# Optimization experiments

Hardware: AMD Instinct MI355X
Metric: run time of the kernel (lower is better)

Reference implementation:

```python
import jax, jax.numpy as jnp
import numpy as np

N_NODES = 100000
N_EDGES = 1600000
FEAT = 128
HID = 128
CLS = 4


def setup_inputs() -> dict:
    key = jax.random.key(0)
    ks = jax.random.split(key, 10)
    x = jax.random.normal(ks[0], (N_NODES, FEAT), dtype=jnp.float32)
    edge_index = jax.random.randint(ks[1], (2, N_EDGES), 0, N_NODES, dtype=jnp.int64)
    s1 = 1.0 / np.sqrt(FEAT)
    s2 = 1.0 / np.sqrt(HID)
    s3 = 1.0 / np.sqrt(CLS)
    return {
        "x": x,
        "edge_index": edge_index,
        "W1l": jax.random.uniform(ks[2], (HID, FEAT), jnp.float32, -s1, s1),
        "b1": jax.random.uniform(ks[3], (HID,), jnp.float32, -s1, s1),
        "W1r": jax.random.uniform(ks[4], (HID, FEAT), jnp.float32, -s1, s1),
        "W2l": jax.random.uniform(ks[5], (CLS, HID), jnp.float32, -s2, s2),
        "b2": jax.random.uniform(ks[6], (CLS,), jnp.float32, -s2, s2),
        "W2r": jax.random.uniform(ks[7], (CLS, HID), jnp.float32, -s2, s2),
        "Wlin": jax.random.uniform(ks[8], (2, CLS), jnp.float32, -s3, s3),
        "blin": jax.random.uniform(ks[9], (2,), jnp.float32, -s3, s3),
    }


def _sage_conv(h, src, dst, Wl, bl, Wr, n_nodes):
    # PyG SAGEConv (mean aggr, root_weight=True): lin_l(mean_j h_j) + lin_r(h_i)
    msg = h[src]  # [E, d] irregular gather
    agg = jax.ops.segment_sum(msg, dst, num_segments=n_nodes)  # [N, d]
    deg = jax.ops.segment_sum(jnp.ones((src.shape[0], 1), h.dtype), dst,
                              num_segments=n_nodes)  # [N, 1]
    agg = agg / jnp.maximum(deg, 1.0)
    return agg @ Wl.T + bl + h @ Wr.T


def reference(x, edge_index, W1l, b1, W1r, W2l, b2, W2r, Wlin, blin):
    n = x.shape[0]
    src, dst = edge_index[0], edge_index[1]
    h = jax.nn.relu(_sage_conv(x, src, dst, W1l, b1, W1r, n))
    # dropout is identity in eval mode (training=False)
    h = _sage_conv(h, src, dst, W2l, b2, W2r, n)  # [N, 4]
    return h @ Wlin.T + blin  # [N, 2]
```

## Files before the change

### kernel.cpp

```cpp
#include <hip/hip_runtime.h>

#define NN 100000
#define NE 1600000
#define NBUK 1563
#define EB 8192

typedef __attribute__((ext_vector_type(8))) short v8s;
typedef __attribute__((ext_vector_type(4))) float v4f;

__device__ __forceinline__ unsigned short f2bf(float f) {
  unsigned int u = __float_as_uint(f);
  unsigned int r = (u + 0x7FFFu + ((u >> 16) & 1u)) >> 16;
  return (unsigned short)r;
}
__device__ __forceinline__ float bflo(unsigned int w) { return __uint_as_float(w << 16); }
__device__ __forceinline__ float bfhi(unsigned int w) { return __uint_as_float(w & 0xFFFF0000u); }
__device__ __forceinline__ float bf2f(unsigned short w) {
  return __uint_as_float((unsigned int)w << 16);
}


__global__ void k_zerob(int* __restrict__ hist) {
  int i = blockIdx.x * blockDim.x + threadIdx.x;
  if (i < NBUK) hist[i] = 0;
}

__global__ __launch_bounds__(256) void k_hist(const int* __restrict__ dst,
                                              int* __restrict__ hist) {
  __shared__ int lh[NBUK];
  int t = threadIdx.x;
  for (int i = t; i < NBUK; i += 256) lh[i] = 0;
  __syncthreads();
  int base = blockIdx.x * 16384;
  int lim = min(16384, NE - base);
  for (int j = t; j < lim; j += 256) atomicAdd(&lh[dst[base + j] >> 6], 1);
  __syncthreads();
  for (int i = t; i < NBUK; i += 256) {
    int c = lh[i];
    if (c) atomicAdd(&hist[i], c);
  }
}

__global__ __launch_bounds__(256) void k_scanb(const int* __restrict__ hist,
                                               int* __restrict__ bbase,
                                               int* __restrict__ gcur) {
  __shared__ int sc[256];
  __shared__ int carry;
  int t = threadIdx.x;
  if (t == 0) carry = 0;
  __syncthreads();
  for (int c = 0; c < (NBUK + 255) / 256; ++c) {
    int i = c * 256 + t;
    int vv = (i < NBUK) ? hist[i] : 0;
    sc[t] = vv;
    __syncthreads();
    for (int o = 1; o < 256; o <<= 1) {
      int uu = (t >= o) ? sc[t - o] : 0;
      __syncthreads();
      sc[t] += uu;
      __syncthreads();
    }
    int excl = carry + sc[t] - vv;
    if (i < NBUK) { bbase[i] = excl; gcur[i] = excl; }
    __syncthreads();
    if (t == 0) carry += sc[255];
    __syncthreads();
  }
}

extern __shared__ char smem_dyn[];
__global__ __launch_bounds__(256) void k_scatter(const int* __restrict__ src,
                                                 const int* __restrict__ dst,
                                                 int* __restrict__ gcur,
                                                 unsigned int* __restrict__ staged) {
  unsigned int* stageP = (unsigned int*)smem_dyn;
  unsigned short* stageB = (unsigned short*)(stageP + EB);
  int* lhist  = (int*)(stageB + EB);
  int* lbase  = lhist + NBUK;
  int* lcur   = lbase + NBUK;
  int* gclaim = lcur + NBUK;
  __shared__ int sc[256];
  __shared__ int carry;
  int t = threadIdx.x;
  int e0 = blockIdx.x * EB;
  int ecnt = min(EB, NE - e0);
  for (int i = t; i < NBUK; i += 256) lhist[i] = 0;
  if (t == 0) carry = 0;
  __syncthreads();
  for (int j = t; j < ecnt; j += 256) atomicAdd(&lhist[dst[e0 + j] >> 6], 1);
  __syncthreads();
  for (int c = 0; c < (NBUK + 255) / 256; ++c) {
    int i = c * 256 + t;
    int vv = (i < NBUK) ? lhist[i] : 0;
    sc[t] = vv;
    __syncthreads();
    for (int o = 1; o < 256; o <<= 1) {
      int uu = (t >= o) ? sc[t - o] : 0;
      __syncthreads();
      sc[t] += uu;
      __syncthreads();
    }
    int excl = carry + sc[t] - vv;
    if (i < NBUK) { lbase[i] = excl; lcur[i] = excl; }
    __syncthreads();
    if (t == 0) carry += sc[255];
    __syncthreads();
  }
  for (int b = t; b < NBUK; b += 256) {
    int c = lhist[b];
    gclaim[b] = c ? atomicAdd(&gcur[b], c) : 0;
  }
  __syncthreads();
  for (int j = t; j < ecnt; j += 256) {
    int s = src[e0 + j], d = dst[e0 + j];
    int b = d >> 6;
    int lp = atomicAdd(&lcur[b], 1);
    stageP[lp] = ((unsigned int)s << 6) | (unsigned int)(d & 63);
    stageB[lp] = (unsigned short)b;
  }
  __syncthreads();
  for (int i = t; i < ecnt; i += 256) {
    int b = stageB[i];
    staged[gclaim[b] + (i - lbase[b])] = stageP[i];
  }
}

__global__ __launch_bounds__(256) void k_sort2(const unsigned int* __restrict__ staged,
                                               const int* __restrict__ bbase,
                                               const int* __restrict__ hist,
                                               int* __restrict__ csr,
                                               int* __restrict__ off,
                                               int* __restrict__ deg) {
  __shared__ int h64[64], c64[64];
  int bkt = blockIdx.x, t = threadIdx.x;
  if (t < 64) h64[t] = 0;
  __syncthreads();
  int st = bbase[bkt], cnt = hist[bkt];
  for (int j = t; j < cnt; j += 256) atomicAdd(&h64[staged[st + j] & 63], 1);
  __syncthreads();
  if (t < 64) {
    int v = h64[t];
    int inc = v;
    for (int o = 1; o < 64; o <<= 1) {
      int uu = __shfl_up(inc, o, 64);
      if (t >= o) inc += uu;
    }
    int excl = inc - v;
    c64[t] = excl;
    int node = bkt * 64 + t;
    if (node < NN) { off[node] = st + excl; deg[node] = v; }
  }
  __syncthreads();
  for (int j = t; j < cnt; j += 256) {
    unsigned pk = staged[st + j];
    int lp = atomicAdd(&c64[pk & 63], 1);
    csr[st + lp] = (int)(pk >> 6);
  }
}


__global__ void k_packw(const float* __restrict__ W1l, const float* __restrict__ W1r,
                        unsigned short* __restrict__ Wcat) {
  int i = blockIdx.x * blockDim.x + threadIdx.x;
  float f = (i < 16384) ? W1l[i] : W1r[i - 16384];
  Wcat[i] = f2bf(f);
}

__global__ __launch_bounds__(256) void k_gemm1(
    const float* __restrict__ x, const unsigned short* __restrict__ Wcat,
    unsigned short* __restrict__ u, unsigned short* __restrict__ v) {
  int wave = threadIdx.x >> 6, l = threadIdx.x & 63;
  int m0 = blockIdx.x * 64 + wave * 16;
  if (m0 >= NN) return;
  int lr = l & 15, kq = l >> 4;
  int rowc = min(m0 + lr, NN - 1);

  v8s a[4];
#pragma unroll
  for (int ks = 0; ks < 4; ++ks) {
    const float* xp = x + (size_t)rowc * 128 + ks * 32 + kq * 8;
    float4 f0 = *(const float4*)xp;
    float4 f1 = *(const float4*)(xp + 4);
    v8s tv;
    tv[0] = (short)f2bf(f0.x); tv[1] = (short)f2bf(f0.y);
    tv[2] = (short)f2bf(f0.z); tv[3] = (short)f2bf(f0.w);
    tv[4] = (short)f2bf(f1.x); tv[5] = (short)f2bf(f1.y);
    tv[6] = (short)f2bf(f1.z); tv[7] = (short)f2bf(f1.w);
    a[ks] = tv;
  }

  v4f acc[16];
#pragma unroll
  for (int nt = 0; nt < 16; ++nt) acc[nt] = (v4f){0.f, 0.f, 0.f, 0.f};

#pragma unroll
  for (int nt = 0; nt < 16; ++nt) {
    const unsigned short* wrow = Wcat + (size_t)(nt * 16 + lr) * 128;
#pragma unroll
    for (int ks = 0; ks < 4; ++ks) {
      v8s b = *(const v8s*)(wrow + ks * 32 + kq * 8);
      acc[nt] = __builtin_amdgcn_mfma_f32_16x16x32_bf16(a[ks], b, acc[nt], 0, 0, 0);
    }
  }

#pragma unroll
  for (int nt = 0; nt < 16; ++nt) {
#pragma unroll
    for (int rr = 0; rr < 4; ++rr) {
      int mrow = m0 + kq * 4 + rr;
      if (mrow < NN) {
        unsigned short bv = f2bf(acc[nt][rr]);
        int col = nt * 16 + lr;
        if (nt < 8) u[(size_t)mrow * 128 + col] = bv;
        else        v[(size_t)mrow * 128 + (col - 128)] = bv;
      }
    }
  }
}

__global__ __launch_bounds__(256) void k_agg(
    const unsigned short* __restrict__ u, const unsigned short* __restrict__ v,
    const int* __restrict__ csr, const int* __restrict__ off, const int* __restrict__ deg,
    const float* __restrict__ b1,
    const float* __restrict__ W2l, const float* __restrict__ W2r,
    float* __restrict__ p, float* __restrict__ r) {
  int wid = (blockIdx.x * blockDim.x + threadIdx.x) >> 6;
  int l = threadIdx.x & 63;
  if (wid >= NN) return;
  int cnt = deg[wid], st = off[wid];
  int half = l >> 5;
  int dpos = l & 31;
  const char* ubase = (const char*)u + (dpos << 3);

  uint2 vw = *(const uint2*)((const char*)v + ((size_t)wid << 8) + (dpos << 3));
  float4 bb = *(const float4*)(b1 + 4 * dpos);
  const float* Wbase = half ? W2r : W2l;
  float4 wv[4];
#pragma unroll
  for (int o = 0; o < 4; ++o) wv[o] = *(const float4*)(Wbase + o * 128 + 4 * dpos);

  float a0 = 0.f, a1 = 0.f, a2 = 0.f, a3 = 0.f;

#define LOADW(W, S) uint2 W = *(const uint2*)(ubase + ((size_t)((unsigned)(S) << 8)))
#define ACCW(W) { a0 += bflo(W.x); a1 += bfhi(W.x); a2 += bflo(W.y); a3 += bfhi(W.y); }

  for (int base = 0; base < cnt; base += 64) {
    int nloc = min(64, cnt - base);
    int idx = 0;
    if (l < nloc) idx = csr[st + base + l];
    int npair = nloc >> 1;
    int e = 0;
    for (; e + 8 <= npair; e += 8) {
      int s0 = __shfl(idx, 2 * e + half, 64);
      int s1 = __shfl(idx, 2 * (e + 1) + half, 64);
      int s2 = __shfl(idx, 2 * (e + 2) + half, 64);
      int s3 = __shfl(idx, 2 * (e + 3) + half, 64);
      int s4 = __shfl(idx, 2 * (e + 4) + half, 64);
      int s5 = __shfl(idx, 2 * (e + 5) + half, 64);
      int s6 = __shfl(idx, 2 * (e + 6) + half, 64);
      int s7 = __shfl(idx, 2 * (e + 7) + half, 64);
      LOADW(w0, s0);
      LOADW(w1, s1);
      LOADW(w2, s2);
      LOADW(w3, s3);
      LOADW(w4, s4);
      LOADW(w5, s5);
      LOADW(w6, s6);
      LOADW(w7, s7);
      ACCW(w0); ACCW(w1); ACCW(w2); ACCW(w3);
      ACCW(w4); ACCW(w5); ACCW(w6); ACCW(w7);
    }
    for (; e + 4 <= npair; e += 4) {
      int s0 = __shfl(idx, 2 * e + half, 64);
      int s1 = __shfl(idx, 2 * (e + 1) + half, 64);
      int s2 = __shfl(idx, 2 * (e + 2) + half, 64);
      int s3 = __shfl(idx, 2 * (e + 3) + half, 64);
      LOADW(w0, s0);
      LOADW(w1, s1);
      LOADW(w2, s2);
      LOADW(w3, s3);
      ACCW(w0); ACCW(w1); ACCW(w2); ACCW(w3);
    }
    for (; e < npair; ++e) {
      int s = __shfl(idx, 2 * e + half, 64);
      LOADW(w, s);
      ACCW(w);
    }
    if (nloc & 1) {
      int s = __shfl(idx, nloc - 1, 64);
      if (half == 0) {
        LOADW(w, s);
        ACCW(w);
      }
    }
  }
#undef LOADW
#undef ACCW

  a0 += __shfl_xor(a0, 32, 64);
  a1 += __shfl_xor(a1, 32, 64);
  a2 += __shfl_xor(a2, 32, 64);
  a3 += __shfl_xor(a3, 32, 64);

  float inv = 1.f / (float)max(cnt, 1);
  float h0 = fmaxf(fmaf(a0, inv, bflo(vw.x) + bb.x), 0.f);
  float h1 = fmaxf(fmaf(a1, inv, bfhi(vw.x) + bb.y), 0.f);
  float h2 = fmaxf(fmaf(a2, inv, bflo(vw.y) + bb.z), 0.f);
  float h3 = fmaxf(fmaf(a3, inv, bfhi(vw.y) + bb.w), 0.f);

  float t0 = h0 * wv[0].x + h1 * wv[0].y + h2 * wv[0].z + h3 * wv[0].w;
  float t1 = h0 * wv[1].x + h1 * wv[1].y + h2 * wv[1].z + h3 * wv[1].w;
  float t2 = h0 * wv[2].x + h1 * wv[2].y + h2 * wv[2].z + h3 * wv[2].w;
  float t3 = h0 * wv[3].x + h1 * wv[3].y + h2 * wv[3].z + h3 * wv[3].w;
  float v01 = (l & 1) ? t1 : t0;
  float w01 = __shfl_xor((l & 1) ? t0 : t1, 1, 64);
  float r01 = v01 + w01;
  float v23 = (l & 1) ? t3 : t2;
  float w23 = __shfl_xor((l & 1) ? t2 : t3, 1, 64);
  float r23 = v23 + w23;
  float vq = (l & 2) ? r23 : r01;
  float wq = __shfl_xor((l & 2) ? r01 : r23, 2, 64);
  float rr = vq + wq;
  rr += __shfl_xor(rr, 4, 64);
  rr += __shfl_xor(rr, 8, 64);
  rr += __shfl_xor(rr, 16, 64);
  float* outp = half ? r : p;
  if (dpos < 4) outp[(size_t)wid * 4 + dpos] = rr;
}

__global__ __launch_bounds__(256) void k_final(
    const float* __restrict__ p, const float* __restrict__ r,
    const int* __restrict__ csr, const int* __restrict__ off,
    const int* __restrict__ deg,
    const float* __restrict__ b2,
    const float* __restrict__ Wlin, const float* __restrict__ blin,
    float* __restrict__ out) {
  int gid = blockIdx.x * blockDim.x + threadIdx.x;
  int node = gid >> 3;
  int sl = gid & 7;
  if (node >= NN) return;
  int cnt = deg[node], st = off[node];
  int l = threadIdx.x & 63;

  float a0 = 0.f, a1 = 0.f, a2 = 0.f, a3 = 0.f;
  for (int e = sl; e < cnt; e += 8) {
    int s = csr[st + e];
    const float4 pv = *(const float4*)(p + (size_t)s * 4);
    a0 += pv.x; a1 += pv.y; a2 += pv.z; a3 += pv.w;
  }
  float v01 = (l & 1) ? a1 : a0;
  float w01 = __shfl_xor((l & 1) ? a0 : a1, 1, 64);
  float r01 = v01 + w01;
  float v23 = (l & 1) ? a3 : a2;
  float w23 = __shfl_xor((l & 1) ? a2 : a3, 1, 64);
  float r23 = v23 + w23;
  float vq = (l & 2) ? r23 : r01;
  float wq = __shfl_xor((l & 2) ? r01 : r23, 2, 64);
  float rr = vq + wq;
  rr += __shfl_xor(rr, 4, 64);
  int o = sl & 3;
  float inv = 1.f / (float)max(cnt, 1);
  float g = rr * inv + b2[o] + r[(size_t)node * 4 + o];
  float t0 = g * Wlin[o];
  float t1 = g * Wlin[4 + o];
  float vv = (l & 1) ? t1 : t0;
  float ww = __shfl_xor((l & 1) ? t0 : t1, 1, 64);
  float q = vv + ww;
  q += __shfl_xor(q, 2, 64);
  if (sl < 2) out[(size_t)node * 2 + sl] = q + blin[sl];
}


extern "C" void kernel_launch(void* const* d_in, const int* in_sizes, int n_in,
                              void* d_out, int out_size, void* d_ws, size_t ws_size,
                              hipStream_t stream) {
  const float* x    = (const float*)d_in[0];
  const int*   ei   = (const int*)d_in[1];
  const int*   src  = ei;
  const int*   dst  = ei + NE;
  const float* W1l  = (const float*)d_in[2];
  const float* b1   = (const float*)d_in[3];
  const float* W1r  = (const float*)d_in[4];
  const float* W2l  = (const float*)d_in[5];
  const float* b2   = (const float*)d_in[6];
  const float* W2r  = (const float*)d_in[7];
  const float* Wlin = (const float*)d_in[8];
  const float* blin = (const float*)d_in[9];
  float* out = (float*)d_out;

  char* w = (char*)d_ws;
  size_t o = 0;
  auto alloc = [&](size_t bytes) {
    void* pp = (void*)(w + o);
    o = (o + bytes + 255) & ~(size_t)255;
    return pp;
  };
  int* hist  = (int*)alloc(NBUK * 4);
  int* bbase = (int*)alloc(NBUK * 4);
  int* gcur  = (int*)alloc(NBUK * 4);
  unsigned int*  staged = (unsigned int*)alloc((size_t)NE * 4);
  int* csr   = (int*)alloc((size_t)NE * 4);
  int* offs  = (int*)alloc(NN * 4);
  int* deg   = (int*)alloc(NN * 4);
  unsigned short* Wcat  = (unsigned short*)alloc(256 * 128 * 2);
  unsigned short* ubuf  = (unsigned short*)alloc((size_t)NN * 128 * 2);
  unsigned short* vbuf  = (unsigned short*)alloc((size_t)NN * 128 * 2);
  float* pbuf = (float*)alloc((size_t)NN * 4 * 4);
  float* rbuf = (float*)alloc((size_t)NN * 4 * 4);

  const size_t scatter_lds = (size_t)EB * 4 + (size_t)EB * 2 + (size_t)4 * NBUK * 4;

  hipLaunchKernelGGL(k_zerob, dim3((NBUK + 255) / 256), dim3(256), 0, stream, hist);
  hipLaunchKernelGGL(k_hist,  dim3((NE + 16383) / 16384), dim3(256), 0, stream, dst, hist);
  hipLaunchKernelGGL(k_scanb, dim3(1), dim3(256), 0, stream, hist, bbase, gcur);
  hipLaunchKernelGGL(k_scatter, dim3((NE + EB - 1) / EB), dim3(256), scatter_lds, stream,
                     src, dst, gcur, staged);
  hipLaunchKernelGGL(k_sort2, dim3(NBUK), dim3(256), 0, stream,
                     staged, bbase, hist, csr, offs, deg);
  hipLaunchKernelGGL(k_packw, dim3(128), dim3(256), 0, stream, W1l, W1r, Wcat);
  hipLaunchKernelGGL(k_gemm1, dim3((NN + 63) / 64), dim3(256), 0, stream, x, Wcat, ubuf, vbuf);
  hipLaunchKernelGGL(k_agg,   dim3((NN * 64 + 255) / 256), dim3(256), 0, stream,
                     ubuf, vbuf, csr, offs, deg, b1, W2l, W2r, pbuf, rbuf);
  hipLaunchKernelGGL(k_final, dim3((NN * 8 + 255) / 256), dim3(256), 0, stream,
                     pbuf, rbuf, csr, offs, deg, b2, Wlin, blin, out);
}
```

Measured before the change: 317.8 us.

## Stage W in LDS for gemm1 and swap MFMA operands for vector stores

The first-layer GEMM now copies the packed 256x128 bf16 weight matrix into padded shared memory once per block, instead of having every wave read it from global memory. The MFMA operands are swapped so each lane holds four consecutive output columns of one row. This lets results be written as packed 8-byte stores rather than scattered 2-byte stores. The cost is about 68KB of LDS per block, which limits occupancy, plus a block barrier; the early return for out-of-range waves is removed.

Result: faster. 281.0 us (-11.6%).

```diff
diff --git a/kernel.cpp b/kernel.cpp
--- a/kernel.cpp
+++ b/kernel.cpp
@@ -169,9 +169,20 @@
 __global__ __launch_bounds__(256) void k_gemm1(
     const float* __restrict__ x, const unsigned short* __restrict__ Wcat,
     unsigned short* __restrict__ u, unsigned short* __restrict__ v) {
-  int wave = threadIdx.x >> 6, l = threadIdx.x & 63;
+  char* wlds = smem_dyn;
+  int t = threadIdx.x;
+  {
+    int rsub = t >> 4, chunk = t & 15;
+#pragma unroll
+    for (int rd = 0; rd < 16; ++rd) {
+      int row = rd * 16 + rsub;
+      uint4 w4 = *(const uint4*)(Wcat + (size_t)row * 128 + chunk * 8);
+      *(uint4*)(wlds + row * 272 + chunk * 16) = w4;
+    }
+  }
+
+  int wave = t >> 6, l = t & 63;
   int m0 = blockIdx.x * 64 + wave * 16;
-  if (m0 >= NN) return;
   int lr = l & 15, kq = l >> 4;
   int rowc = min(m0 + lr, NN - 1);
 
@@ -189,31 +200,31 @@
     a[ks] = tv;
   }
 
+  __syncthreads();
+
   v4f acc[16];
 #pragma unroll
   for (int nt = 0; nt < 16; ++nt) acc[nt] = (v4f){0.f, 0.f, 0.f, 0.f};
 
 #pragma unroll
   for (int nt = 0; nt < 16; ++nt) {
-    const unsigned short* wrow = Wcat + (size_t)(nt * 16 + lr) * 128;
+    const char* wrow = wlds + (nt * 16 + lr) * 272;
 #pragma unroll
     for (int ks = 0; ks < 4; ++ks) {
-      v8s b = *(const v8s*)(wrow + ks * 32 + kq * 8);
-      acc[nt] = __builtin_amdgcn_mfma_f32_16x16x32_bf16(a[ks], b, acc[nt], 0, 0, 0);
-    }
-  }
-
-#pragma unroll
-  for (int nt = 0; nt < 16; ++nt) {
-#pragma unroll
-    for (int rr = 0; rr < 4; ++rr) {
-      int mrow = m0 + kq * 4 + rr;
-      if (mrow < NN) {
-        unsigned short bv = f2bf(acc[nt][rr]);
-        int col = nt * 16 + lr;
-        if (nt < 8) u[(size_t)mrow * 128 + col] = bv;
-        else        v[(size_t)mrow * 128 + (col - 128)] = bv;
-      }
+      v8s b = *(const v8s*)(wrow + ks * 64 + kq * 16);
+      acc[nt] = __builtin_amdgcn_mfma_f32_16x16x32_bf16(b, a[ks], acc[nt], 0, 0, 0);
+    }
+  }
+
+  if (m0 + lr < NN) {
+    size_t rowb = (size_t)(m0 + lr) * 128;
+#pragma unroll
+    for (int nt = 0; nt < 16; ++nt) {
+      unsigned lo = (unsigned)f2bf(acc[nt][0]) | ((unsigned)f2bf(acc[nt][1]) << 16);
+      unsigned hi = (unsigned)f2bf(acc[nt][2]) | ((unsigned)f2bf(acc[nt][3]) << 16);
+      int col = (nt & 7) * 16 + kq * 4;
+      if (nt < 8) *(uint2*)(u + rowb + col) = make_uint2(lo, hi);
+      else        *(uint2*)(v + rowb + col) = make_uint2(lo, hi);
     }
   }
 }
@@ -409,6 +420,7 @@
   float* rbuf = (float*)alloc((size_t)NN * 4 * 4);
 
   const size_t scatter_lds = (size_t)EB * 4 + (size_t)EB * 2 + (size_t)4 * NBUK * 4;
+  const size_t gemm1_lds = 256 * 272;
 
   hipLaunchKernelGGL(k_zerob, dim3((NBUK + 255) / 256), dim3(256), 0, stream, hist);
   hipLaunchKernelGGL(k_hist,  dim3((NE + 16383) / 16384), dim3(256), 0, stream, dst, hist);
@@ -418,7 +430,8 @@
   hipLaunchKernelGGL(k_sort2, dim3(NBUK), dim3(256), 0, stream,
                      staged, bbase, hist, csr, offs, deg);
   hipLaunchKernelGGL(k_packw, dim3(128), dim3(256), 0, stream, W1l, W1r, Wcat);
-  hipLaunchKernelGGL(k_gemm1, dim3((NN + 63) / 64), dim3(256), 0, stream, x, Wcat, ubuf, vbuf);
+  hipLaunchKernelGGL(k_gemm1, dim3((NN + 63) / 64), dim3(256), gemm1_lds, stream,
+                     x, Wcat, ubuf, vbuf);
   hipLaunchKernelGGL(k_agg,   dim3((NN * 64 + 255) / 256), dim3(256), 0, stream,
                      ubuf, vbuf, csr, offs, deg, b1, W2l, W2r, pbuf, rbuf);
   hipLaunchKernelGGL(k_final, dim3((NN * 8 + 255) / 256), dim3(256), 0, stream,
```
